# Kernel tuning notes

Hardware: AMD Instinct MI355X
Metric: run time of the kernel (lower is better)

Reference implementation:

```python
import jax, jax.numpy as jnp
import numpy as np

NEG_INF = -1e30
EPS = 1e-7  # keras epsilon used by K.ctc_batch_cost


def setup_inputs() -> dict:
    key = jax.random.key(0)
    k1, k2 = jax.random.split(key)
    B, T, C, L = 1024, 256, 128, 32
    logits = jax.random.normal(k1, (B, T, C), dtype=jnp.float32)
    y_pred = jax.nn.softmax(logits, axis=-1)  # ctc_batch_cost expects probabilities
    y_true = jax.random.randint(k2, (B, L), 0, 126, dtype=jnp.int64)
    return {"y_true": y_true, "y_pred": y_pred}


def _ctc_batch_cost(y_true, y_pred):
    # Faithful to K.ctc_batch_cost with input_length=T, label_length=L, blank=C-1
    B, T, C = y_pred.shape
    L = y_true.shape[1]
    blank = C - 1
    S = 2 * L + 1
    logp = jnp.log(y_pred + EPS)  # [B,T,C]

    # extended label sequence: blank, l0, blank, l1, ..., blank  -> [B,S]
    ext = jnp.full((B, S), blank, dtype=jnp.int32)
    ext = ext.at[:, 1::2].set(y_true.astype(jnp.int32))

    # emission log-probs along extended labels: [B,T,S]
    lp_ext = jnp.take_along_axis(logp, ext[:, None, :], axis=2)

    # s-2 skip allowed only for non-blank labels differing from label two back
    is_blank = ext == blank
    same2 = jnp.concatenate(
        [jnp.ones((B, 2), bool), ext[:, 2:] == ext[:, :-2]], axis=1)
    skip_add = jnp.where(is_blank | same2, NEG_INF, 0.0)  # [B,S]

    alpha0 = jnp.full((B, S), NEG_INF, dtype=logp.dtype)
    alpha0 = alpha0.at[:, 0].set(lp_ext[:, 0, 0])
    alpha0 = alpha0.at[:, 1].set(lp_ext[:, 0, 1])

    def shift(x, n):
        return jnp.pad(x, ((0, 0), (n, 0)), constant_values=NEG_INF)[:, :S]

    def step(alpha, lp_t):
        a0 = alpha
        a1 = shift(alpha, 1)
        a2 = jnp.maximum(shift(alpha, 2) + skip_add, NEG_INF)
        m = jnp.maximum(jnp.maximum(a0, a1), a2)
        lse = m + jnp.log(jnp.exp(a0 - m) + jnp.exp(a1 - m) + jnp.exp(a2 - m))
        new = jnp.maximum(lse + lp_t, NEG_INF)
        return new, None

    lp_ext_t = jnp.swapaxes(lp_ext, 0, 1)  # [T,B,S]
    alpha_T, _ = jax.lax.scan(step, alpha0, lp_ext_t[1:])
    final = jnp.logaddexp(alpha_T[:, S - 1], alpha_T[:, S - 2])  # [B]
    return -final[:, None]  # [B,1] like ctc_batch_cost


def reference(y_true, y_pred):
    return _ctc_batch_cost(y_true, y_pred)
```

## Files before the change

kernel.cpp:

```cpp
#include <hip/hip_runtime.h>
#include <hip/hip_bf16.h>


#define CTC_B 1024
#define CTC_T 256
#define CTC_C 128
#define CTC_L 32
#define CTC_BLANK 127
#define CTC_EPS 1e-7f

#define RSTRIDE 34

#define DPP_WAVE_SHL1 0x130
#define DPP_WAVE_SHR1 0x138

__device__ __forceinline__ double bperm_f64(int addr, double v) {
    union { double d; int i[2]; } u; u.d = v;
    int x = __builtin_amdgcn_ds_bpermute(addr, u.i[0]);
    int y = __builtin_amdgcn_ds_bpermute(addr, u.i[1]);
    union { int i[2]; double d; } r; r.i[0] = x; r.i[1] = y;
    return r.d;
}

__device__ __forceinline__ double dpp_shr1_f64(double v) {
    union { double d; int i[2]; } u; u.d = v;
    int x = __builtin_amdgcn_update_dpp(0, u.i[0], DPP_WAVE_SHR1, 0xF, 0xF, true);
    int y = __builtin_amdgcn_update_dpp(0, u.i[1], DPP_WAVE_SHR1, 0xF, 0xF, true);
    union { int i[2]; double d; } r; r.i[0] = x; r.i[1] = y;
    return r.d;
}

__device__ __forceinline__ double dpp_shl1_f64(double v) {
    union { double d; int i[2]; } u; u.d = v;
    int x = __builtin_amdgcn_update_dpp(0, u.i[0], DPP_WAVE_SHL1, 0xF, 0xF, true);
    int y = __builtin_amdgcn_update_dpp(0, u.i[1], DPP_WAVE_SHL1, 0xF, 0xF, true);
    union { int i[2]; double d; } r; r.i[0] = x; r.i[1] = y;
    return r.d;
}

__device__ __forceinline__ double bcast0_f64(double v) {
    union { double d; int i[2]; } u; u.d = v;
    int x = __builtin_amdgcn_readfirstlane(u.i[0]);
    int y = __builtin_amdgcn_readfirstlane(u.i[1]);
    union { int i[2]; double d; } r; r.i[0] = x; r.i[1] = y;
    return r.d;
}

__global__ __launch_bounds__(256) void ctc_loss_kernel(
    const int* __restrict__ y_true,
    const float* __restrict__ y_pred,
    float* __restrict__ out)
{
    __shared__ float lp[CTC_T * RSTRIDE];

    const int b = blockIdx.x;
    const int tid = threadIdx.x;
    const int lane = tid & 63;
    const int wave = tid >> 6;

    const float* yp = y_pred + (size_t)b * CTC_T * CTC_C;

    int lbl = CTC_BLANK;
    if (lane < CTC_L) lbl = y_true[b * CTC_L + lane];

    {
        const int t0 = wave * 64;
        const int src_addr = (lbl >> 1) << 2;
        const bool odd = (lbl & 1) != 0;
        #pragma unroll 8
        for (int k = 0; k < 64; ++k) {
            const int t = t0 + k;
            const float2 r =
                *reinterpret_cast<const float2*>(yp + (size_t)t * CTC_C + 2 * lane);
            union { float f; int i; } c0, c1;
            c0.f = r.x; c1.f = r.y;
            int g0 = __builtin_amdgcn_ds_bpermute(src_addr, c0.i);
            int g1 = __builtin_amdgcn_ds_bpermute(src_addr, c1.i);
            union { int i; float f; } s0, s1;
            s0.i = g0; s1.i = g1;
            float p = odd ? s1.f : s0.f;
            float v = (lane == 33) ? 0.0f : (p + CTC_EPS) * 128.0f;
            if (lane <= 33) lp[t * RSTRIDE + lane] = v;
        }
    }
    __syncthreads();

    if (wave != 0) return;

    double skip = 0.0;
    if (lane >= 1 && lane < CTC_L) {
        if (y_true[b * CTC_L + lane - 1] != lbl) skip = 1.0;
    }
    double skipn = 0.0;
    if (lane <= 30) {
        if (y_true[b * CTC_L + lane + 1] != lbl) skipn = 1.0;
    } else if (lane == 32) {
        skipn = 1.0;
    }

    const int lidx = (lane < 32) ? lane : 32;
    const int pv_idx = (lane < 32) ? lane : 33;
    const int tn = (lane <= 30) ? (lane + 1)
                 : (lane == 31) ? 33
                 : (lane == 32) ? 0
                 : 32;
    const int pbi = (lane == 32) ? 33 : 32;

    const bool is32 = (lane == 32);

    double lo = 0.0, hi = 0.0;
    if (lane == 0) {
        lo = (double)lp[32];
        hi = (double)lp[0];
    }
    double a = 0.0, bb = 0.0;
    if (lane == 31) { a = 1.0; bb = 1.0; }

    #pragma unroll 4
    for (int k = 0; k < 127; ++k) {
        const int tf = 1 + k;
        const int tb = 255 - k;
        float pvf  = lp[tf * RSTRIDE + pv_idx];
        float pbf  = lp[tf * RSTRIDE + 32];
        float paf  = lp[tb * RSTRIDE + lidx];
        float pa1f = lp[tb * RSTRIDE + tn];
        float pbbf = lp[tb * RSTRIDE + pbi];

        double ph  = dpp_shr1_f64(hi);
        double a1s = dpp_shl1_f64(a);
        double a1  = is32 ? bcast0_f64(a) : a1s;

        double nl = (lo + ph) * (double)pbf;
        double nh = (hi + lo + skip * ph) * (double)pvf;
        double v  = (double)pa1f * a1;
        double u  = (double)pbbf * bb;
        double nb = u + v;
        double na = fma((double)paf, a, fma(skipn, v, u));

        lo = nl; hi = nh; a = na; bb = nb;
    }

    {
        const int tb = 128;
        float paf  = lp[tb * RSTRIDE + lidx];
        float pa1f = lp[tb * RSTRIDE + tn];
        float pbbf = lp[tb * RSTRIDE + pbi];
        double a1s = dpp_shl1_f64(a);
        double a1  = is32 ? bcast0_f64(a) : a1s;
        double v  = (double)pa1f * a1;
        double u  = (double)pbbf * bb;
        double nb = u + v;
        double na = fma((double)paf, a, fma(skipn, v, u));
        a = na; bb = nb;
    }

    double beA = bperm_f64(32 << 2, a);
    double beB = bperm_f64(((lane + 63) & 63) << 2, bb);
    double be = (lane == 0) ? beA : beB;
    double partial = (lane <= 32) ? (lo * be + hi * a) : 0.0;
    #pragma unroll
    for (int off = 32; off >= 1; off >>= 1)
        partial += __shfl_down(partial, off);
    if (lane == 0) {
        out[b] = (float)(1242.1197475634219 - log(partial));
    }
}

extern "C" void kernel_launch(void* const* d_in, const int* in_sizes, int n_in,
                              void* d_out, int out_size, void* d_ws, size_t ws_size,
                              hipStream_t stream) {
    const int*   y_true = (const int*)d_in[0];
    const float* y_pred = (const float*)d_in[1];
    float*       out    = (float*)d_out;

    ctc_loss_kernel<<<CTC_B, 256, 0, stream>>>(y_true, y_pred, out);
}
```

Baseline: 210.0 us.

## Transpose LDS emission tables to label-major and prefetch vectorized per-step loads

Stores emission probabilities in two label-major LDS tables (forward and reversed backward time order), so each lane reads consecutive time steps contiguously. The recurrence loop then loads four steps at a time with float2 reads and double-buffers the next group ahead of the current four steps. This is meant to cut the number of LDS load instructions on the serial recurrence path and hide their latency. The cost is more registers, plus strided LDS writes in the staging phase, which may cause bank conflicts.

```diff
diff --git a/kernel.cpp b/kernel.cpp
--- a/kernel.cpp
+++ b/kernel.cpp
@@ -9,7 +9,8 @@
 #define CTC_BLANK 127
 #define CTC_EPS 1e-7f
 
-#define RSTRIDE 34
+#define KSTRIDE 130
+#define TABSZ  (34 * KSTRIDE)
 
 #define DPP_WAVE_SHL1 0x130
 #define DPP_WAVE_SHR1 0x138
@@ -51,7 +52,9 @@
     const float* __restrict__ y_pred,
     float* __restrict__ out)
 {
-    __shared__ float lp[CTC_T * RSTRIDE];
+    __shared__ float tabs[2 * TABSZ];
+    float* Ftab = tabs;
+    float* Btab = tabs + TABSZ;
 
     const int b = blockIdx.x;
     const int tid = threadIdx.x;
@@ -67,6 +70,7 @@
         const int t0 = wave * 64;
         const int src_addr = (lbl >> 1) << 2;
         const bool odd = (lbl & 1) != 0;
+        float* tab = (wave < 2) ? Ftab : Btab;
         #pragma unroll 8
         for (int k = 0; k < 64; ++k) {
             const int t = t0 + k;
@@ -80,7 +84,8 @@
             s0.i = g0; s1.i = g1;
             float p = odd ? s1.f : s0.f;
             float v = (lane == 33) ? 0.0f : (p + CTC_EPS) * 128.0f;
-            if (lane <= 33) lp[t * RSTRIDE + lane] = v;
+            const int idx = (wave < 2) ? ((t + 127) & 127) : (255 - t);
+            if (lane <= 33) tab[lane * KSTRIDE + idx] = v;
         }
     }
     __syncthreads();
@@ -105,54 +110,79 @@
                  : (lane == 32) ? 0
                  : 32;
     const int pbi = (lane == 32) ? 33 : 32;
-
     const bool is32 = (lane == 32);
+
+    const float* Fpv = Ftab + pv_idx * KSTRIDE;
+    const float* Fpb = Ftab + 32 * KSTRIDE;
+    const float* Bpa = Btab + lidx * KSTRIDE;
+    const float* Bp1 = Btab + tn * KSTRIDE;
+    const float* Bpb = Btab + pbi * KSTRIDE;
 
     double lo = 0.0, hi = 0.0;
     if (lane == 0) {
-        lo = (double)lp[32];
-        hi = (double)lp[0];
+        lo = (double)Ftab[32 * KSTRIDE + 127];
+        hi = (double)Ftab[0 * KSTRIDE + 127];
     }
     double a = 0.0, bb = 0.0;
     if (lane == 31) { a = 1.0; bb = 1.0; }
 
-    #pragma unroll 4
-    for (int k = 0; k < 127; ++k) {
-        const int tf = 1 + k;
-        const int tb = 255 - k;
-        float pvf  = lp[tf * RSTRIDE + pv_idx];
-        float pbf  = lp[tf * RSTRIDE + 32];
-        float paf  = lp[tb * RSTRIDE + lidx];
-        float pa1f = lp[tb * RSTRIDE + tn];
-        float pbbf = lp[tb * RSTRIDE + pbi];
-
-        double ph  = dpp_shr1_f64(hi);
+#define STEP(pvf, pbf, paf, pa1f, pbbf) {                       \
+        double ph  = dpp_shr1_f64(hi);                          \
+        double a1s = dpp_shl1_f64(a);                           \
+        double a1  = is32 ? bcast0_f64(a) : a1s;                \
+        double nl = (lo + ph) * (double)(pbf);                  \
+        double nh = (hi + lo + skip * ph) * (double)(pvf);      \
+        double v  = (double)(pa1f) * a1;                        \
+        double u  = (double)(pbbf) * bb;                        \
+        double nb = u + v;                                      \
+        double na = fma((double)(paf), a, fma(skipn, v, u));    \
+        lo = nl; hi = nh; a = na; bb = nb;                      \
+    }
+
+#define LD2(p, o) (*reinterpret_cast<const float2*>((p) + (o)))
+
+    float2 c_pv0 = LD2(Fpv, 0), c_pv1 = LD2(Fpv, 2);
+    float2 c_pb0 = LD2(Fpb, 0), c_pb1 = LD2(Fpb, 2);
+    float2 c_pa0 = LD2(Bpa, 0), c_pa1 = LD2(Bpa, 2);
+    float2 c_p10 = LD2(Bp1, 0), c_p11 = LD2(Bp1, 2);
+    float2 c_pb0b = LD2(Bpb, 0), c_pb1b = LD2(Bpb, 2);
+
+    for (int g = 0; g < 31; ++g) {
+        const int o = 4 * (g + 1);
+        float2 n_pv0 = LD2(Fpv, o), n_pv1 = LD2(Fpv, o + 2);
+        float2 n_pb0 = LD2(Fpb, o), n_pb1 = LD2(Fpb, o + 2);
+        float2 n_pa0 = LD2(Bpa, o), n_pa1 = LD2(Bpa, o + 2);
+        float2 n_p10 = LD2(Bp1, o), n_p11 = LD2(Bp1, o + 2);
+        float2 n_pb0b = LD2(Bpb, o), n_pb1b = LD2(Bpb, o + 2);
+
+        STEP(c_pv0.x, c_pb0.x, c_pa0.x, c_p10.x, c_pb0b.x);
+        STEP(c_pv0.y, c_pb0.y, c_pa0.y, c_p10.y, c_pb0b.y);
+        STEP(c_pv1.x, c_pb1.x, c_pa1.x, c_p11.x, c_pb1b.x);
+        STEP(c_pv1.y, c_pb1.y, c_pa1.y, c_p11.y, c_pb1b.y);
+
+        c_pv0 = n_pv0; c_pv1 = n_pv1;
+        c_pb0 = n_pb0; c_pb1 = n_pb1;
+        c_pa0 = n_pa0; c_pa1 = n_pa1;
+        c_p10 = n_p10; c_p11 = n_p11;
+        c_pb0b = n_pb0b; c_pb1b = n_pb1b;
+    }
+
+    STEP(c_pv0.x, c_pb0.x, c_pa0.x, c_p10.x, c_pb0b.x);
+    STEP(c_pv0.y, c_pb0.y, c_pa0.y, c_p10.y, c_pb0b.y);
+    STEP(c_pv1.x, c_pb1.x, c_pa1.x, c_p11.x, c_pb1b.x);
+
+    {
         double a1s = dpp_shl1_f64(a);
         double a1  = is32 ? bcast0_f64(a) : a1s;
-
-        double nl = (lo + ph) * (double)pbf;
-        double nh = (hi + lo + skip * ph) * (double)pvf;
-        double v  = (double)pa1f * a1;
-        double u  = (double)pbbf * bb;
+        double v  = (double)c_p11.y * a1;
+        double u  = (double)c_pb1b.y * bb;
         double nb = u + v;
-        double na = fma((double)paf, a, fma(skipn, v, u));
-
-        lo = nl; hi = nh; a = na; bb = nb;
-    }
-
-    {
-        const int tb = 128;
-        float paf  = lp[tb * RSTRIDE + lidx];
-        float pa1f = lp[tb * RSTRIDE + tn];
-        float pbbf = lp[tb * RSTRIDE + pbi];
-        double a1s = dpp_shl1_f64(a);
-        double a1  = is32 ? bcast0_f64(a) : a1s;
-        double v  = (double)pa1f * a1;
-        double u  = (double)pbbf * bb;
-        double nb = u + v;
-        double na = fma((double)paf, a, fma(skipn, v, u));
+        double na = fma((double)c_pa1.y, a, fma(skipn, v, u));
         a = na; bb = nb;
     }
+
+#undef STEP
+#undef LD2
 
     double beA = bperm_f64(32 << 2, a);
     double beB = bperm_f64(((lane + 63) & 63) << 2, bb);
```

Result: no change. 212.5 us (+1.2%).
